# Optimization experiments

Measured on AMD Instinct MI355X. Metric: run time of the kernel, lower is better.

Reference implementation:

```python
import jax, jax.numpy as jnp
import numpy as np

B, C, H, W = 128, 3, 512, 512
P, NP, SCALE = 16, 3, 2          # patch_size, num_patches, scale
HG, HL = 256, 128                # hidden_g, hidden_l
D_IN = NP * C * P * P            # 2304


def _extract_patch(x, coords, size):
    # x: (B,C,H,W), coords: (B,2) int [x_coord, y_coord]; returns (B,C,size,size)
    pad = size // 2
    xp = jnp.pad(x, ((0, 0), (0, 0), (pad, pad), (pad, pad)))
    ch = xp.shape[1]

    def one(img, c):
        # slice [from_y:from_y+size, from_x:from_x+size]
        return jax.lax.dynamic_slice(img, (0, c[1], c[0]), (ch, size, size))

    return jax.vmap(one)(xp, coords)


def _foveate(x, l):
    h, w = x.shape[2], x.shape[3]
    # torch uses l.data (detached) and .long() truncation; values are >= 0
    coords = (0.5 * ((jax.lax.stop_gradient(l) + 1.0)
                     * jnp.array([h, w], jnp.float32))).astype(jnp.int32)
    patches = []
    size = P
    for _ in range(NP):
        p = _extract_patch(x, coords, size)
        if size > P:
            k = size // P  # avg_pool2d kernel = stride = k
            b, c = p.shape[0], p.shape[1]
            p = p.reshape(b, c, P, k, P, k).mean(axis=(3, 5))
        patches.append(p)
        size = int(SCALE * size)
    g = jnp.concatenate(patches, axis=1)  # (B, NP*C, P, P)
    return g.reshape(g.shape[0], -1)      # (B, D_IN)


def setup_inputs() -> dict:
    key = jax.random.key(0)
    ks = jax.random.split(key, 10)
    s = 0.02
    return {
        "x_t": jax.random.normal(ks[0], (B, C, H, W), jnp.float32),
        "l_t": jax.random.uniform(ks[1], (B, 2), jnp.float32, -1.0, 1.0),
        "w1": jax.random.normal(ks[2], (D_IN, HG), jnp.float32) * s,
        "b1": jnp.zeros((HG,), jnp.float32),
        "w2": jax.random.normal(ks[3], (2, HL), jnp.float32) * s,
        "b2": jnp.zeros((HL,), jnp.float32),
        "w3": jax.random.normal(ks[4], (HG, HG + HL), jnp.float32) * s,
        "b3": jnp.zeros((HG + HL,), jnp.float32),
        "w4": jax.random.normal(ks[5], (HL, HG + HL), jnp.float32) * s,
        "b4": jnp.zeros((HG + HL,), jnp.float32),
    }


def reference(x_t, l_t, w1, b1, w2, b2, w3, b3, w4, b4):
    glimpse = _foveate(x_t, l_t)                       # (B, D_IN)
    what = jax.nn.relu(glimpse @ w1 + b1) @ w3 + b3    # (B, HG+HL)
    where = jax.nn.relu(l_t @ w2 + b2) @ w4 + b4       # (B, HG+HL)
    return jax.nn.relu(what + where)
```

## Files before the change

kernel.cpp:

```cpp
#include <hip/hip_runtime.h>
#include <hip/hip_bf16.h>


#define B_    128
#define C_    3
#define H_    512
#define W_    512
#define P_    16
#define HG    256
#define HL    128
#define DIN   2304
#define HOUT  384

#define KS 36
#define BK 64
#define BM 32
#define BN 64

__global__ __launch_bounds__(256) void k1_foveate(
    const float* __restrict__ x, const float* __restrict__ l,
    float* __restrict__ glimpse)
{
    __shared__ float ld[64 * 64];
    const int bid = blockIdx.x;
    const int b = bid / C_;
    const int c = bid % C_;
    const int t = threadIdx.x;

    const float l0 = l[b * 2 + 0];
    const float l1 = l[b * 2 + 1];
    const int sx = (int)(((l0 + 1.0f) * 512.0f) * 0.5f);
    const int sy = (int)(((l1 + 1.0f) * 512.0f) * 0.5f);

    const float* xc = x + (size_t)(b * C_ + c) * (H_ * W_);

    for (int f = t; f < 64 * 64; f += 256) {
        const int r  = f >> 6;
        const int cc = f & 63;
        const int ry = sy - 32 + r;
        const int rx = sx - 32 + cc;
        ld[f] = (ry >= 0 && ry < H_ && rx >= 0 && rx < W_) ? xc[ry * W_ + rx] : 0.0f;
    }
    __syncthreads();

    const int py = t >> 4;
    const int px = t & 15;

    const float v0 = ld[(24 + py) * 64 + 24 + px];

    float s1 = 0.0f;
    #pragma unroll
    for (int dy = 0; dy < 2; ++dy) {
        const float2 v = *(const float2*)&ld[(16 + 2 * py + dy) * 64 + 16 + 2 * px];
        s1 += v.x + v.y;
    }

    float s2 = 0.0f;
    #pragma unroll
    for (int dy = 0; dy < 4; ++dy) {
        const float4 v = *(const float4*)&ld[(py * 4 + dy) * 64 + px * 4];
        s2 += v.x + v.y + v.z + v.w;
    }

    float* g = glimpse + (size_t)b * DIN;
    g[(0 * C_ + c) * 256 + t] = v0;
    g[(1 * C_ + c) * 256 + t] = s1 * 0.25f;
    g[(2 * C_ + c) * 256 + t] = s2 * 0.0625f;
}

__global__ __launch_bounds__(256) void k2_gemm1(
    const float* __restrict__ glimpse, const float* __restrict__ w1,
    float* __restrict__ partial)
{
    __shared__ float As[BM][BK + 4];
    __shared__ float Bs[BK][BN];

    const int bid = blockIdx.x;
    const int ks  = bid % KS;
    const int jb  = bid / KS;
    const int jt  = jb & 3;
    const int bt  = jb >> 2;
    const int t   = threadIdx.x;
    const int k0  = ks * BK;

    {
        int f = t;
        int row = f >> 4, c4 = f & 15;
        float4 v = *(const float4*)&glimpse[(size_t)(bt * BM + row) * DIN + k0 + c4 * 4];
        *(float4*)&As[row][c4 * 4] = v;
        f = t + 256;
        row = f >> 4; c4 = f & 15;
        float4 v2 = *(const float4*)&glimpse[(size_t)(bt * BM + row) * DIN + k0 + c4 * 4];
        *(float4*)&As[row][c4 * 4] = v2;
    }
    #pragma unroll
    for (int i = 0; i < 4; ++i) {
        const int f  = t + 256 * i;
        const int kr = f >> 4, c4 = f & 15;
        float4 v = *(const float4*)&w1[(size_t)(k0 + kr) * HG + jt * BN + c4 * 4];
        *(float4*)&Bs[kr][c4 * 4] = v;
    }
    __syncthreads();

    const int tx = t & 15;
    const int ty = t >> 4;
    float4 acc0 = {0.f, 0.f, 0.f, 0.f};
    float4 acc1 = {0.f, 0.f, 0.f, 0.f};
    #pragma unroll 8
    for (int k = 0; k < BK; ++k) {
        const float a0 = As[ty][k];
        const float a1 = As[ty + 16][k];
        const float4 bv = *(const float4*)&Bs[k][tx * 4];
        acc0.x += a0 * bv.x; acc0.y += a0 * bv.y; acc0.z += a0 * bv.z; acc0.w += a0 * bv.w;
        acc1.x += a1 * bv.x; acc1.y += a1 * bv.y; acc1.z += a1 * bv.z; acc1.w += a1 * bv.w;
    }
    float* p0 = &partial[((size_t)(ks * B_ + bt * BM + ty)) * HG + jt * BN + tx * 4];
    *(float4*)p0 = acc0;
    float* p1 = &partial[((size_t)(ks * B_ + bt * BM + ty + 16)) * HG + jt * BN + tx * 4];
    *(float4*)p1 = acc1;
}

__global__ __launch_bounds__(384) void k3_out(
    const float* __restrict__ partial, const float* __restrict__ b1,
    const float* __restrict__ w3, const float* __restrict__ b3,
    const float* __restrict__ l,  const float* __restrict__ w2,
    const float* __restrict__ b2, const float* __restrict__ w4,
    const float* __restrict__ b4, float* __restrict__ out)
{
    __shared__ float hs[HG];
    __shared__ float hl[HL];
    const int b = blockIdx.x;
    const int t = threadIdx.x;

    if (t < HG) {
        float a0 = 0.f, a1 = 0.f, a2 = 0.f, a3 = 0.f;
        #pragma unroll
        for (int s = 0; s < KS; s += 4) {
            a0 += partial[((size_t)((s + 0) * B_ + b)) * HG + t];
            a1 += partial[((size_t)((s + 1) * B_ + b)) * HG + t];
            a2 += partial[((size_t)((s + 2) * B_ + b)) * HG + t];
            a3 += partial[((size_t)((s + 3) * B_ + b)) * HG + t];
        }
        hs[t] = fmaxf((a0 + a1) + (a2 + a3) + b1[t], 0.0f);
    } else if (t < HG + HL) {
        const int j = t - HG;
        const float l0 = l[b * 2 + 0];
        const float l1 = l[b * 2 + 1];
        hl[j] = fmaxf(l0 * w2[j] + l1 * w2[HL + j] + b2[j], 0.0f);
    }
    __syncthreads();

    float acc = b3[t] + b4[t];
    #pragma unroll 8
    for (int i = 0; i < HG; ++i)
        acc += hs[i] * w3[i * HOUT + t];
    #pragma unroll 8
    for (int i = 0; i < HL; ++i)
        acc += hl[i] * w4[i * HOUT + t];
    out[(size_t)b * HOUT + t] = fmaxf(acc, 0.0f);
}

extern "C" void kernel_launch(void* const* d_in, const int* in_sizes, int n_in,
                              void* d_out, int out_size, void* d_ws, size_t ws_size,
                              hipStream_t stream) {
    const float* x_t = (const float*)d_in[0];
    const float* l_t = (const float*)d_in[1];
    const float* w1  = (const float*)d_in[2];
    const float* b1  = (const float*)d_in[3];
    const float* w2  = (const float*)d_in[4];
    const float* b2  = (const float*)d_in[5];
    const float* w3  = (const float*)d_in[6];
    const float* b3  = (const float*)d_in[7];
    const float* w4  = (const float*)d_in[8];
    const float* b4  = (const float*)d_in[9];
    float* out = (float*)d_out;

    float* ws      = (float*)d_ws;
    float* glimpse = ws;
    float* partial = glimpse + (size_t)B_ * DIN;

    k1_foveate<<<B_ * C_, 256, 0, stream>>>(x_t, l_t, glimpse);
    k2_gemm1<<<16 * KS, 256, 0, stream>>>(glimpse, w1, partial);
    k3_out<<<B_, 384, 0, stream>>>(partial, b1, w3, b3, l_t, w2, b2, w4, b4, out);
}
```

Baseline: 483.8 us.

## Fuse foveation, first GEMM and output layer into one per-sample kernel

Replaces the three-kernel pipeline (patch extraction, split-K tiled GEMM, reduction plus output layer) with a single kernel where each block handles one batch sample. The glimpse stays in shared memory and the first layer becomes a per-block GEMV split across two halves of K, so the glimpse and partial-sum global buffers and two launches disappear. In exchange, every block streams all of w1 from cache, parallelism drops to 128 blocks, and the tiled register reuse of the old GEMM is lost.

```diff
diff --git a/kernel.cpp b/kernel.cpp
--- a/kernel.cpp
+++ b/kernel.cpp
@@ -1,30 +1,31 @@
 #include <hip/hip_runtime.h>
-#include <hip/hip_bf16.h>
 
 
 #define B_    128
 #define C_    3
 #define H_    512
 #define W_    512
-#define P_    16
 #define HG    256
 #define HL    128
 #define DIN   2304
 #define HOUT  384
+#define NT    512
 
-#define KS 36
-#define BK 64
-#define BM 32
-#define BN 64
+__global__ __launch_bounds__(NT) void glimpse_fused(
+    const float* __restrict__ x,  const float* __restrict__ l,
+    const float* __restrict__ w1, const float* __restrict__ b1,
+    const float* __restrict__ w2, const float* __restrict__ b2,
+    const float* __restrict__ w3, const float* __restrict__ b3,
+    const float* __restrict__ w4, const float* __restrict__ b4,
+    float* __restrict__ out)
+{
+    __shared__ float ld[C_ * 64 * 64];
+    __shared__ float g[DIN];
+    __shared__ float red[NT];
+    __shared__ float hs[HG];
+    __shared__ float hl[HL];
 
-__global__ __launch_bounds__(256) void k1_foveate(
-    const float* __restrict__ x, const float* __restrict__ l,
-    float* __restrict__ glimpse)
-{
-    __shared__ float ld[64 * 64];
-    const int bid = blockIdx.x;
-    const int b = bid / C_;
-    const int c = bid % C_;
+    const int b = blockIdx.x;
     const int t = threadIdx.x;
 
     const float l0 = l[b * 2 + 0];
@@ -32,137 +33,90 @@
     const int sx = (int)(((l0 + 1.0f) * 512.0f) * 0.5f);
     const int sy = (int)(((l1 + 1.0f) * 512.0f) * 0.5f);
 
-    const float* xc = x + (size_t)(b * C_ + c) * (H_ * W_);
+    const float* xb = x + (size_t)b * (C_ * H_ * W_);
 
-    for (int f = t; f < 64 * 64; f += 256) {
-        const int r  = f >> 6;
+    for (int f = t; f < C_ * 4096; f += NT) {
+        const int c  = f >> 12;
+        const int r  = (f >> 6) & 63;
         const int cc = f & 63;
         const int ry = sy - 32 + r;
         const int rx = sx - 32 + cc;
-        ld[f] = (ry >= 0 && ry < H_ && rx >= 0 && rx < W_) ? xc[ry * W_ + rx] : 0.0f;
+        ld[f] = (ry >= 0 && ry < H_ && rx >= 0 && rx < W_)
+                    ? xb[c * (H_ * W_) + ry * W_ + rx] : 0.0f;
     }
     __syncthreads();
 
-    const int py = t >> 4;
-    const int px = t & 15;
-
-    const float v0 = ld[(24 + py) * 64 + 24 + px];
-
-    float s1 = 0.0f;
-    #pragma unroll
-    for (int dy = 0; dy < 2; ++dy) {
-        const float2 v = *(const float2*)&ld[(16 + 2 * py + dy) * 64 + 16 + 2 * px];
-        s1 += v.x + v.y;
-    }
-
-    float s2 = 0.0f;
-    #pragma unroll
-    for (int dy = 0; dy < 4; ++dy) {
-        const float4 v = *(const float4*)&ld[(py * 4 + dy) * 64 + px * 4];
-        s2 += v.x + v.y + v.z + v.w;
-    }
-
-    float* g = glimpse + (size_t)b * DIN;
-    g[(0 * C_ + c) * 256 + t] = v0;
-    g[(1 * C_ + c) * 256 + t] = s1 * 0.25f;
-    g[(2 * C_ + c) * 256 + t] = s2 * 0.0625f;
-}
-
-__global__ __launch_bounds__(256) void k2_gemm1(
-    const float* __restrict__ glimpse, const float* __restrict__ w1,
-    float* __restrict__ partial)
-{
-    __shared__ float As[BM][BK + 4];
-    __shared__ float Bs[BK][BN];
-
-    const int bid = blockIdx.x;
-    const int ks  = bid % KS;
-    const int jb  = bid / KS;
-    const int jt  = jb & 3;
-    const int bt  = jb >> 2;
-    const int t   = threadIdx.x;
-    const int k0  = ks * BK;
-
-    {
-        int f = t;
-        int row = f >> 4, c4 = f & 15;
-        float4 v = *(const float4*)&glimpse[(size_t)(bt * BM + row) * DIN + k0 + c4 * 4];
-        *(float4*)&As[row][c4 * 4] = v;
-        f = t + 256;
-        row = f >> 4; c4 = f & 15;
-        float4 v2 = *(const float4*)&glimpse[(size_t)(bt * BM + row) * DIN + k0 + c4 * 4];
-        *(float4*)&As[row][c4 * 4] = v2;
-    }
-    #pragma unroll
-    for (int i = 0; i < 4; ++i) {
-        const int f  = t + 256 * i;
-        const int kr = f >> 4, c4 = f & 15;
-        float4 v = *(const float4*)&w1[(size_t)(k0 + kr) * HG + jt * BN + c4 * 4];
-        *(float4*)&Bs[kr][c4 * 4] = v;
+    for (int idx = t; idx < DIN; idx += NT) {
+        const int pos   = idx & 255;
+        const int cl    = idx >> 8;
+        const int level = cl / 3;
+        const int c     = cl - level * 3;
+        const int py    = pos >> 4;
+        const int px    = pos & 15;
+        const float* pc = ld + c * 4096;
+        float v;
+        if (level == 0) {
+            v = pc[(24 + py) * 64 + 24 + px];
+        } else if (level == 1) {
+            float s = 0.0f;
+            #pragma unroll
+            for (int dy = 0; dy < 2; ++dy) {
+                const float2 u = *(const float2*)&pc[(16 + 2 * py + dy) * 64 + 16 + 2 * px];
+                s += u.x + u.y;
+            }
+            v = s * 0.25f;
+        } else {
+            float s = 0.0f;
+            #pragma unroll
+            for (int dy = 0; dy < 4; ++dy) {
+                const float4 u = *(const float4*)&pc[(4 * py + dy) * 64 + 4 * px];
+                s += (u.x + u.y) + (u.z + u.w);
+            }
+            v = s * 0.0625f;
+        }
+        g[idx] = v;
     }
     __syncthreads();
 
-    const int tx = t & 15;
-    const int ty = t >> 4;
-    float4 acc0 = {0.f, 0.f, 0.f, 0.f};
-    float4 acc1 = {0.f, 0.f, 0.f, 0.f};
-    #pragma unroll 8
-    for (int k = 0; k < BK; ++k) {
-        const float a0 = As[ty][k];
-        const float a1 = As[ty + 16][k];
-        const float4 bv = *(const float4*)&Bs[k][tx * 4];
-        acc0.x += a0 * bv.x; acc0.y += a0 * bv.y; acc0.z += a0 * bv.z; acc0.w += a0 * bv.w;
-        acc1.x += a1 * bv.x; acc1.y += a1 * bv.y; acc1.z += a1 * bv.z; acc1.w += a1 * bv.w;
+    {
+        const int j    = t & 255;
+        const int half = t >> 8;
+        const float* gp = g  + half * 1152;
+        const float* wp = w1 + half * 1152 * HG + j;
+        float a0 = 0.f, a1 = 0.f, a2 = 0.f, a3 = 0.f;
+        #pragma unroll 2
+        for (int k = 0; k < 1152; k += 4) {
+            a0 += gp[k + 0] * wp[(k + 0) * HG];
+            a1 += gp[k + 1] * wp[(k + 1) * HG];
+            a2 += gp[k + 2] * wp[(k + 2) * HG];
+            a3 += gp[k + 3] * wp[(k + 3) * HG];
+        }
+        red[t] = (a0 + a1) + (a2 + a3);
     }
-    float* p0 = &partial[((size_t)(ks * B_ + bt * BM + ty)) * HG + jt * BN + tx * 4];
-    *(float4*)p0 = acc0;
-    float* p1 = &partial[((size_t)(ks * B_ + bt * BM + ty + 16)) * HG + jt * BN + tx * 4];
-    *(float4*)p1 = acc1;
-}
-
-__global__ __launch_bounds__(384) void k3_out(
-    const float* __restrict__ partial, const float* __restrict__ b1,
-    const float* __restrict__ w3, const float* __restrict__ b3,
-    const float* __restrict__ l,  const float* __restrict__ w2,
-    const float* __restrict__ b2, const float* __restrict__ w4,
-    const float* __restrict__ b4, float* __restrict__ out)
-{
-    __shared__ float hs[HG];
-    __shared__ float hl[HL];
-    const int b = blockIdx.x;
-    const int t = threadIdx.x;
+    __syncthreads();
 
     if (t < HG) {
-        float a0 = 0.f, a1 = 0.f, a2 = 0.f, a3 = 0.f;
-        #pragma unroll
-        for (int s = 0; s < KS; s += 4) {
-            a0 += partial[((size_t)((s + 0) * B_ + b)) * HG + t];
-            a1 += partial[((size_t)((s + 1) * B_ + b)) * HG + t];
-            a2 += partial[((size_t)((s + 2) * B_ + b)) * HG + t];
-            a3 += partial[((size_t)((s + 3) * B_ + b)) * HG + t];
-        }
-        hs[t] = fmaxf((a0 + a1) + (a2 + a3) + b1[t], 0.0f);
+        hs[t] = fmaxf(red[t] + red[t + 256] + b1[t], 0.0f);
     } else if (t < HG + HL) {
         const int j = t - HG;
-        const float l0 = l[b * 2 + 0];
-        const float l1 = l[b * 2 + 1];
         hl[j] = fmaxf(l0 * w2[j] + l1 * w2[HL + j] + b2[j], 0.0f);
     }
     __syncthreads();
 
-    float acc = b3[t] + b4[t];
-    #pragma unroll 8
-    for (int i = 0; i < HG; ++i)
-        acc += hs[i] * w3[i * HOUT + t];
-    #pragma unroll 8
-    for (int i = 0; i < HL; ++i)
-        acc += hl[i] * w4[i * HOUT + t];
-    out[(size_t)b * HOUT + t] = fmaxf(acc, 0.0f);
+    if (t < HOUT) {
+        float acc = b3[t] + b4[t];
+        #pragma unroll 8
+        for (int i = 0; i < HG; ++i) acc += hs[i] * w3[i * HOUT + t];
+        #pragma unroll 8
+        for (int i = 0; i < HL; ++i) acc += hl[i] * w4[i * HOUT + t];
+        out[(size_t)b * HOUT + t] = fmaxf(acc, 0.0f);
+    }
 }
 
 extern "C" void kernel_launch(void* const* d_in, const int* in_sizes, int n_in,
                               void* d_out, int out_size, void* d_ws, size_t ws_size,
                               hipStream_t stream) {
+    (void)d_ws; (void)ws_size; (void)in_sizes; (void)n_in; (void)out_size;
     const float* x_t = (const float*)d_in[0];
     const float* l_t = (const float*)d_in[1];
     const float* w1  = (const float*)d_in[2];
@@ -173,13 +127,7 @@
     const float* b3  = (const float*)d_in[7];
     const float* w4  = (const float*)d_in[8];
     const float* b4  = (const float*)d_in[9];
-    float* out = (float*)d_out;
 
-    float* ws      = (float*)d_ws;
-    float* glimpse = ws;
-    float* partial = glimpse + (size_t)B_ * DIN;
-
-    k1_foveate<<<B_ * C_, 256, 0, stream>>>(x_t, l_t, glimpse);
-    k2_gemm1<<<16 * KS, 256, 0, stream>>>(glimpse, w1, partial);
-    k3_out<<<B_, 384, 0, stream>>>(partial, b1, w3, b3, l_t, w2, b2, w4, b4, out);
+    glimpse_fused<<<B_, NT, 0, stream>>>(x_t, l_t, w1, b1, w2, b2, w3, b3, w4, b4,
+                                         (float*)d_out);
 }
```

Measured after the change: 540.9 us. 1.12x slower.
